# Kernel optimization log

Hardware: AMD Instinct MI355X
Metric: run time of the kernel (lower is better)

The kernel has to match this reference:

```python
import jax, jax.numpy as jnp
import numpy as np

EMBED = 2048
HEADS = 16
HEAD_DIM = EMBED // HEADS


def setup_inputs() -> dict:
    key = jax.random.key(0)
    ks = jax.random.split(key, 9)
    B, S, E = 4, 2048, EMBED
    scale = 1.0 / np.sqrt(E)
    return {
        "values": jax.random.normal(ks[0], (B, S, E), jnp.float32),
        "keys": jax.random.normal(ks[1], (B, S, E), jnp.float32),
        "query": jax.random.normal(ks[2], (B, S, E), jnp.float32),
        "mask": jax.random.randint(ks[3], (1, 1, S, S), 0, 2, jnp.int32),
        "Wv": jax.random.normal(ks[4], (E, E), jnp.float32) * scale,
        "Wk": jax.random.normal(ks[5], (E, E), jnp.float32) * scale,
        "Wq": jax.random.normal(ks[6], (E, E), jnp.float32) * scale,
        "Wo": jax.random.normal(ks[7], (E, E), jnp.float32) * scale,
        "bo": jax.random.normal(ks[8], (E,), jnp.float32) * 0.01,
    }


def reference(values, keys, query, mask, Wv, Wk, Wq, Wo, bo):
    N, q_len, E = query.shape
    # QKV projections (no bias)
    v = jnp.matmul(values, Wv)
    k = jnp.matmul(keys, Wk)
    q = jnp.matmul(query, Wq)
    # [N, len, E] -> [N, heads, len, head_dim]
    def split_heads(x):
        return jnp.transpose(x.reshape(N, x.shape[1], HEADS, HEAD_DIM), (0, 2, 1, 3))
    v, k, q = split_heads(v), split_heads(k), split_heads(q)
    # scaled dot-product attention: [N, H, q_len, k_len]
    energy = jnp.einsum("bhqd,bhkd->bhqk", q, k) / jnp.sqrt(jnp.float32(HEAD_DIM))
    energy = jnp.where(mask == 0, jnp.float32(-1e20), energy)
    attn = jax.nn.softmax(energy, axis=-1)
    out = jnp.einsum("bhqk,bhkd->bhqd", attn, v)
    out = jnp.transpose(out, (0, 2, 1, 3)).reshape(N, q_len, E)
    return jnp.matmul(out, Wo) + bo
```

## Files before the change

### kernel.cpp

```cpp
#include <hip/hip_runtime.h>
#include <hip/hip_bf16.h>
#include <stdint.h>
#include <math.h>

#define EMB   2048
#define NH    16
#define HD    128
#define BATCH 4
#define SEQ   2048

typedef __bf16 bf16_t;
typedef __bf16 bf16x8 __attribute__((ext_vector_type(8)));
typedef __bf16 bf16x4 __attribute__((ext_vector_type(4)));
typedef float  f32x4  __attribute__((ext_vector_type(4)));
typedef float  f32x16 __attribute__((ext_vector_type(16)));

__device__ inline void gload_lds16(const void* g, void* l) {
  __builtin_amdgcn_global_load_lds(
      (const __attribute__((address_space(1))) uint32_t*)g,
      (__attribute__((address_space(3))) uint32_t*)l, 16, 0, 0);
}

__device__ inline uint32_t pack_bf2(float a, float b) {
  uint16_t lo = __builtin_bit_cast(uint16_t, (bf16_t)a);
  uint16_t hi = __builtin_bit_cast(uint16_t, (bf16_t)b);
  return (uint32_t)lo | ((uint32_t)hi << 16);
}

__device__ inline float ex2(float x) {
#if __has_builtin(__builtin_amdgcn_exp2f)
  return __builtin_amdgcn_exp2f(x);
#else
  float r; asm volatile("v_exp_f32 %0, %1" : "=v"(r) : "v"(x)); return r;
#endif
}

__device__ inline uint32_t sext1(uint32_t x, int b) {
  return (uint32_t)(((int32_t)(x << (31 - b))) >> 31);
}
__device__ inline float andf(float p, uint32_t m) {
  return __builtin_bit_cast(float, __builtin_bit_cast(uint32_t, p) & m);
}


__global__ __launch_bounds__(256) void conv_bf16(const float* __restrict__ x,
                                                 bf16_t* __restrict__ y) {
  size_t t = (size_t)blockIdx.x * 256 + threadIdx.x;
  float4 v = ((const float4*)x)[t];
  bf16x4 o;
  o[0] = (bf16_t)v.x; o[1] = (bf16_t)v.y; o[2] = (bf16_t)v.z; o[3] = (bf16_t)v.w;
  ((bf16x4*)y)[t] = o;
}

__global__ __launch_bounds__(256) void convT_w(const float* __restrict__ W,
                                               bf16_t* __restrict__ Wt) {
  __shared__ float t[32][33];
  int tx = threadIdx.x & 31, ty = threadIdx.x >> 5;
  int nb = blockIdx.x * 32, kb = blockIdx.y * 32;
#pragma unroll
  for (int i = 0; i < 4; ++i)
    t[ty + 8 * i][tx] = W[(size_t)(kb + ty + 8 * i) * EMB + nb + tx];
  __syncthreads();
#pragma unroll
  for (int i = 0; i < 4; ++i)
    Wt[(size_t)(nb + ty + 8 * i) * EMB + kb + tx] = (bf16_t)t[tx][ty + 8 * i];
}

__global__ __launch_bounds__(256) void pack_mask(const int* __restrict__ mask,
                                                 uint32_t* __restrict__ maskb) {
  int t = blockIdx.x * 256 + threadIdx.x;
  int q = t >> 6, w = t & 63;
  const int* row = mask + (size_t)q * SEQ + w * 32;
  uint32_t acc = 0;
#pragma unroll 8
  for (int i = 0; i < 32; ++i) acc |= (row[i] != 0 ? 1u : 0u) << i;
  maskb[t] = acc;
}

#define KTILES (EMB / 64)

template <int MODE>
__global__ __launch_bounds__(512, 2) void gemm256(const bf16_t* __restrict__ A,
                                                  const bf16_t* __restrict__ Bt,
                                                  bf16_t* __restrict__ outb,
                                                  float* __restrict__ outf,
                                                  const float* __restrict__ bias) {
  extern __shared__ bf16_t lds[];
  const int tid = threadIdx.x;
  const int wid = tid >> 6, lane = tid & 63;
  const int wr = wid >> 2;
  const int wcn = wid & 3;
  const int tn = blockIdx.x & 7;
  const int tm = blockIdx.x >> 3;
  const int m0 = tm * 256, n0 = tn * 256;

  f32x4 acc[8][4] = {};
  bf16x8 af0[4][2], af1[4][2], bfrg[4][2];

  const int trow = tid >> 3;
  const int schunk = ((tid & 7) ^ (trow & 7)) * 8;
  const int fr = lane & 15;
  const int l7 = lane & 7;
  const int hi4 = lane >> 4;
  int cslot[2];
  cslot[0] = ((hi4) ^ l7) * 8;
  cslot[1] = ((4 + hi4) ^ l7) * 8;
  const int arow = wr * 128 + fr;
  const int brow = wcn * 64 + fr;

#define STAGE_HALF(DST, SRC)                                                    \
  do {                                                                          \
    gload_lds16((SRC), &lds[(DST) + wid * 512]);                                \
    gload_lds16((SRC) + (size_t)64 * EMB, &lds[(DST) + wid * 512 + 4096]);      \
  } while (0)

#define STAGE_TILE(B, KT)                                                       \
  do {                                                                          \
    const bf16_t* _a = A + (size_t)(m0 + trow) * EMB + (KT) * 64 + schunk;      \
    STAGE_HALF((B) * 16384, _a);                                                \
    STAGE_HALF((B) * 16384 + 8192, _a + (size_t)128 * EMB);                     \
    const bf16_t* _b = Bt + (size_t)(n0 + trow) * EMB + (KT) * 64 + schunk;     \
    STAGE_HALF(32768 + (B) * 16384, _b);                                        \
    STAGE_HALF(32768 + (B) * 16384 + 8192, _b + (size_t)128 * EMB);             \
  } while (0)

#define READ_A(DST, P, QM)                                                      \
  _Pragma("unroll") for (int i = 0; i < 4; ++i)                                 \
  _Pragma("unroll") for (int ks = 0; ks < 2; ++ks)                              \
    DST[i][ks] = *(const bf16x8*)&lds[(P) * 16384 +                             \
                    (arow + ((QM) * 4 + i) * 16) * 64 + cslot[ks]];

#define READ_B_ALL(P)                                                           \
  _Pragma("unroll") for (int nf = 0; nf < 4; ++nf)                              \
  _Pragma("unroll") for (int ks = 0; ks < 2; ++ks)                              \
    bfrg[nf][ks] = *(const bf16x8*)&lds[32768 + (P) * 16384 +                   \
                    (brow + nf * 16) * 64 + cslot[ks]];

#define MFMA_HALF(SRC, QM)                                                      \
    _Pragma("unroll") for (int i = 0; i < 4; ++i)                               \
    _Pragma("unroll") for (int nf = 0; nf < 4; ++nf)                            \
    _Pragma("unroll") for (int ks = 0; ks < 2; ++ks) {                          \
      if (MODE == 1)                                                            \
        acc[(QM) * 4 + i][nf] = __builtin_amdgcn_mfma_f32_16x16x32_bf16(        \
            bfrg[nf][ks], SRC[i][ks], acc[(QM) * 4 + i][nf], 0, 0, 0);          \
      else                                                                      \
        acc[(QM) * 4 + i][nf] = __builtin_amdgcn_mfma_f32_16x16x32_bf16(        \
            SRC[i][ks], bfrg[nf][ks], acc[(QM) * 4 + i][nf], 0, 0, 0);          \
    }

#define ITER_MAIN(T, P)                                                         \
  do {                                                                          \
    READ_B_ALL(P);                                                              \
    READ_A(af0, P, 0);                                                          \
    READ_A(af1, P, 1);                                                          \
    __builtin_amdgcn_s_setprio(1);                                              \
    MFMA_HALF(af0, 0)                                                           \
    MFMA_HALF(af1, 1)                                                           \
    __builtin_amdgcn_s_setprio(0);                                              \
    asm volatile("s_barrier" ::: "memory");                                     \
    STAGE_TILE(P, (T) + 2);                                                     \
    asm volatile("s_waitcnt vmcnt(8)" ::: "memory");                            \
    asm volatile("s_barrier" ::: "memory");                                     \
  } while (0)

#define ITER_TAIL(P, LAST)                                                      \
  do {                                                                          \
    READ_B_ALL(P);                                                              \
    READ_A(af0, P, 0);                                                          \
    READ_A(af1, P, 1);                                                          \
    __builtin_amdgcn_s_setprio(1);                                              \
    MFMA_HALF(af0, 0)                                                           \
    MFMA_HALF(af1, 1)                                                           \
    __builtin_amdgcn_s_setprio(0);                                              \
    if (!(LAST)) {                                                              \
      asm volatile("s_waitcnt vmcnt(0)" ::: "memory");                          \
      asm volatile("s_barrier" ::: "memory");                                   \
    }                                                                           \
  } while (0)

  STAGE_TILE(0, 0);
  STAGE_TILE(1, 1);
  asm volatile("s_waitcnt vmcnt(8)" ::: "memory");
  asm volatile("s_barrier" ::: "memory");

  for (int t = 0; t < KTILES - 2; t += 2) {
    ITER_MAIN(t, 0);
    ITER_MAIN(t + 1, 1);
  }
  ITER_TAIL(0, 0);
  ITER_TAIL(1, 1);
#undef ITER_TAIL
#undef ITER_MAIN
#undef MFMA_HALF
#undef READ_B_ALL
#undef READ_A
#undef STAGE_TILE
#undef STAGE_HALF

  const int col0 = lane & 15;
  const int row0 = (lane >> 4) * 4;
#pragma unroll
  for (int mf = 0; mf < 8; ++mf) {
#pragma unroll
    for (int r = 0; r < 4; ++r) {
#pragma unroll
      for (int nf = 0; nf < 4; ++nf) {
        float v = acc[mf][nf][r];
        if (MODE == 1) {
          int nr = n0 + wcn * 64 + nf * 16 + row0 + r;
          int mc = m0 + wr * 128 + mf * 16 + col0;
          int b = mc >> 11, s = mc & 2047, h = nr >> 7, d = nr & 127;
          outb[((size_t)(b * NH + h) * HD + d) * SEQ + s] = (bf16_t)v;
        } else {
          int m = m0 + wr * 128 + mf * 16 + row0 + r;
          int n = n0 + wcn * 64 + nf * 16 + col0;
          if (MODE == 0) {
            int b = m >> 11, s = m & 2047, h = n >> 7, d = n & 127;
            outb[((size_t)(b * NH + h) * SEQ + s) * HD + d] = (bf16_t)v;
          } else {
            outf[(size_t)m * EMB + n] = v + bias[n];
          }
        }
      }
    }
  }
}

__global__ __launch_bounds__(256, 2) void attn_fwd(const bf16_t* __restrict__ Q,
                                                   const bf16_t* __restrict__ K,
                                                   const bf16_t* __restrict__ Vt,
                                                   const uint32_t* __restrict__ maskb,
                                                   bf16_t* __restrict__ O) {
  __shared__ bf16_t Ks[2][64 * 128];
  __shared__ bf16_t Vs[2][128 * 64];
  const int tid = threadIdx.x;
  const int wid = tid >> 6, lane = tid & 63;
  const int ln = lane & 31, hi = lane >> 5;
  const int bid = blockIdx.x;
  const int slot = bid >> 3;
  const int bh = (bid & 7) * 8 + (slot >> 4);
  const int qt = slot & 15;
  const int b = bh >> 4, h = bh & 15;
  const int q = qt * 128 + wid * 32 + ln;
  const float C2 = 0.08838834764831845f * 1.4426950408889634f;

  bf16x8 qf[8];
  const bf16_t* qrow = Q + ((size_t)bh * SEQ + q) * HD;
#pragma unroll
  for (int ks = 0; ks < 8; ++ks)
    qf[ks] = *(const bf16x8*)&qrow[ks * 16 + hi * 8];

  const bf16_t* kp[8];
  const bf16_t* vp[4];
#pragma unroll
  for (int ks = 0; ks < 8; ++ks)
    kp[ks] = &Ks[0][ln * 128 + (((2 * ks + hi) ^ (ln & 15)) * 8)];
#pragma unroll
  for (int ks = 0; ks < 4; ++ks)
    vp[ks] = &Vs[0][ln * 64 + (((2 * ks + hi) ^ (ln & 7)) * 8)];

  f32x16 oacc[4] = {};
  float mC = -INFINITY, l_run = 0.f;

  const size_t kbase = (size_t)bh * SEQ * HD;
  const size_t vbase = (size_t)bh * HD * SEQ;
  const uint2* mb = (const uint2*)maskb;

#define STAGE(BUF, KT)                                                          \
  do {                                                                          \
    const int _k0 = (KT) * 64;                                                  \
    _Pragma("unroll")                                                           \
    for (int j = 0; j < 4; ++j) {                                               \
      int i = wid * 4 + j;                                                      \
      { int r = i * 4 + (lane >> 4); int c = lane & 15;                         \
        gload_lds16(&K[kbase + (size_t)(_k0 + r) * HD + ((c ^ (r & 15)) * 8)],  \
                    &Ks[BUF][i * 512]); }                                       \
      { int r = i * 8 + (lane >> 3); int c = lane & 7;                          \
        gload_lds16(&Vt[vbase + (size_t)r * SEQ + _k0 + ((c ^ (r & 7)) * 8)],   \
                    &Vs[BUF][i * 512]); }                                       \
    }                                                                           \
  } while (0)

  const int NT = SEQ / 64;
  uint2 mw_cur = mb[(size_t)q * 32];
  uint2 mw_next;
  STAGE(0, 0);

#define TILE(KT, P)                                                             \
  {                                                                             \
    asm volatile("s_waitcnt vmcnt(0)" ::: "memory");                            \
    asm volatile("s_barrier" ::: "memory");                                     \
    if ((KT) + 1 < NT) {                                                        \
      mw_next = mb[(size_t)q * 32 + (KT) + 1];                                  \
      STAGE((P) ^ 1, (KT) + 1);                                                 \
    }                                                                           \
    f32x16 sacc0 = {}, sacc1 = {};                                              \
    __builtin_amdgcn_s_setprio(1);                                              \
    _Pragma("unroll")                                                           \
    for (int ks = 0; ks < 8; ++ks) {                                            \
      bf16x8 kf0 = *(const bf16x8*)(kp[ks] + (P) * 8192);                       \
      bf16x8 kf1 = *(const bf16x8*)(kp[ks] + 4096 + (P) * 8192);                \
      sacc0 = __builtin_amdgcn_mfma_f32_32x32x16_bf16(kf0, qf[ks], sacc0, 0, 0, 0); \
      sacc1 = __builtin_amdgcn_mfma_f32_32x32x16_bf16(kf1, qf[ks], sacc1, 0, 0, 0); \
    }                                                                           \
    __builtin_amdgcn_s_setprio(0);                                              \
    const uint32_t mwx = mw_cur.x >> (4 * hi);                                  \
    const uint32_t mwy = mw_cur.y >> (4 * hi);                                  \
    float pmax = -INFINITY;                                                     \
    _Pragma("unroll")                                                           \
    for (int r = 0; r < 16; r += 4)                                             \
      pmax = fmaxf(pmax, fmaxf(fmaxf(sacc0[r], sacc0[r + 1]),                   \
                               fmaxf(sacc0[r + 2], sacc0[r + 3])));             \
    _Pragma("unroll")                                                           \
    for (int r = 0; r < 16; r += 4)                                             \
      pmax = fmaxf(pmax, fmaxf(fmaxf(sacc1[r], sacc1[r + 1]),                   \
                               fmaxf(sacc1[r + 2], sacc1[r + 3])));             \
    pmax = fmaxf(pmax, __shfl_xor(pmax, 32, 64));                               \
    const float pmaxC = pmax * C2;                                              \
    if (!__all(pmaxC - mC <= 8.0f)) {                                           \
      const float mnewC = fmaxf(mC, pmaxC);                                     \
      const float corr = ex2(mC - mnewC);                                       \
      _Pragma("unroll")                                                         \
      for (int mv = 0; mv < 4; ++mv)                                            \
        _Pragma("unroll")                                                       \
        for (int r = 0; r < 16; ++r) oacc[mv][r] *= corr;                       \
      l_run *= corr;                                                            \
      mC = mnewC;                                                               \
    }                                                                           \
    const float nmC = -mC;                                                      \
    float psum = 0.f;                                                           \
    uint32_t pk[2][4][2];                                                       \
    _Pragma("unroll")                                                           \
    for (int g = 0; g < 4; ++g) {                                               \
      float p0 = andf(ex2(fmaf(sacc0[4 * g + 0], C2, nmC)), sext1(mwx, 8 * g + 0)); \
      float p1 = andf(ex2(fmaf(sacc0[4 * g + 1], C2, nmC)), sext1(mwx, 8 * g + 1)); \
      float p2 = andf(ex2(fmaf(sacc0[4 * g + 2], C2, nmC)), sext1(mwx, 8 * g + 2)); \
      float p3 = andf(ex2(fmaf(sacc0[4 * g + 3], C2, nmC)), sext1(mwx, 8 * g + 3)); \
      psum += (p0 + p1) + (p2 + p3);                                            \
      pk[0][g][0] = pack_bf2(p0, p1);                                           \
      pk[0][g][1] = pack_bf2(p2, p3);                                           \
      float q0 = andf(ex2(fmaf(sacc1[4 * g + 0], C2, nmC)), sext1(mwy, 8 * g + 0)); \
      float q1 = andf(ex2(fmaf(sacc1[4 * g + 1], C2, nmC)), sext1(mwy, 8 * g + 1)); \
      float q2 = andf(ex2(fmaf(sacc1[4 * g + 2], C2, nmC)), sext1(mwy, 8 * g + 2)); \
      float q3 = andf(ex2(fmaf(sacc1[4 * g + 3], C2, nmC)), sext1(mwy, 8 * g + 3)); \
      psum += (q0 + q1) + (q2 + q3);                                            \
      pk[1][g][0] = pack_bf2(q0, q1);                                           \
      pk[1][g][1] = pack_bf2(q2, q3);                                           \
    }                                                                           \
    psum += __shfl_xor(psum, 32, 64);                                           \
    l_run += psum;                                                              \
    _Pragma("unroll")                                                           \
    for (int ks = 0; ks < 4; ++ks) {                                            \
      const int mfp = ks >> 1;                                                  \
      const int gA = (2 * ks) & 3;                                              \
      uint32_t w0 = pk[mfp][gA][0], w1 = pk[mfp][gA][1];                        \
      uint32_t w2 = pk[mfp][gA + 1][0], w3 = pk[mfp][gA + 1][1];                \
      asm("v_permlane32_swap_b32 %0, %1" : "+v"(w0), "+v"(w2));                 \
      asm("v_permlane32_swap_b32 %0, %1" : "+v"(w1), "+v"(w3));                 \
      uint4 bw = make_uint4(w0, w1, w2, w3);                                    \
      bf16x8 pb = __builtin_bit_cast(bf16x8, bw);                               \
      __builtin_amdgcn_s_setprio(1);                                            \
      _Pragma("unroll")                                                         \
      for (int mv = 0; mv < 4; ++mv) {                                          \
        bf16x8 vf = *(const bf16x8*)(vp[ks] + mv * 2048 + (P) * 8192);          \
        oacc[mv] = __builtin_amdgcn_mfma_f32_32x32x16_bf16(vf, pb, oacc[mv], 0, 0, 0); \
      }                                                                         \
      __builtin_amdgcn_s_setprio(0);                                            \
    }                                                                           \
    mw_cur = mw_next;                                                           \
  }

  for (int t = 0; t < NT; t += 2) {
    TILE(t, 0);
    TILE(t + 1, 1);
  }
#undef TILE
#undef STAGE

  const float invl = 1.f / l_run;
  bf16_t* orow = O + ((size_t)b * SEQ + q) * EMB + h * HD;
#pragma unroll
  for (int mv = 0; mv < 4; ++mv) {
#pragma unroll
    for (int g = 0; g < 4; ++g) {
      int d = mv * 32 + 8 * g + 4 * hi;
      bf16x4 ov;
      ov[0] = (bf16_t)(oacc[mv][4 * g + 0] * invl);
      ov[1] = (bf16_t)(oacc[mv][4 * g + 1] * invl);
      ov[2] = (bf16_t)(oacc[mv][4 * g + 2] * invl);
      ov[3] = (bf16_t)(oacc[mv][4 * g + 3] * invl);
      *(bf16x4*)&orow[d] = ov;
    }
  }
}


extern "C" void kernel_launch(void* const* d_in, const int* in_sizes, int n_in,
                              void* d_out, int out_size, void* d_ws, size_t ws_size,
                              hipStream_t stream) {
  const float* values = (const float*)d_in[0];
  const float* keys   = (const float*)d_in[1];
  const float* query  = (const float*)d_in[2];
  const int*   mask   = (const int*)d_in[3];
  const float* Wv = (const float*)d_in[4];
  const float* Wk = (const float*)d_in[5];
  const float* Wq = (const float*)d_in[6];
  const float* Wo = (const float*)d_in[7];
  const float* bo = (const float*)d_in[8];
  float* out = (float*)d_out;

  char* ws = (char*)d_ws;
  bf16_t*   Xbuf  = (bf16_t*)(ws);
  bf16_t*   Wbuf  = (bf16_t*)(ws + 33554432);
  bf16_t*   Qb    = (bf16_t*)(ws + 41943040);
  bf16_t*   Kb    = (bf16_t*)(ws + 75497472);
  bf16_t*   Vtb   = (bf16_t*)(ws + 109051904);
  uint32_t* maskb = (uint32_t*)(ws + 142606336);

  static const size_t GEMM_LDS = 131072;
  hipFuncSetAttribute(reinterpret_cast<const void*>(gemm256<0>),
                      hipFuncAttributeMaxDynamicSharedMemorySize, (int)GEMM_LDS);
  hipFuncSetAttribute(reinterpret_cast<const void*>(gemm256<1>),
                      hipFuncAttributeMaxDynamicSharedMemorySize, (int)GEMM_LDS);
  hipFuncSetAttribute(reinterpret_cast<const void*>(gemm256<2>),
                      hipFuncAttributeMaxDynamicSharedMemorySize, (int)GEMM_LDS);

  dim3 b256(256), b512(512);
  dim3 gconv(16384);
  dim3 gw(64, 64);
  dim3 gg(256);
  dim3 ga(1024);

  pack_mask<<<dim3(512), b256, 0, stream>>>(mask, maskb);

  conv_bf16<<<gconv, b256, 0, stream>>>(query, Xbuf);
  convT_w<<<gw, b256, 0, stream>>>(Wq, Wbuf);
  gemm256<0><<<gg, b512, GEMM_LDS, stream>>>(Xbuf, Wbuf, Qb, nullptr, nullptr);

  conv_bf16<<<gconv, b256, 0, stream>>>(keys, Xbuf);
  convT_w<<<gw, b256, 0, stream>>>(Wk, Wbuf);
  gemm256<0><<<gg, b512, GEMM_LDS, stream>>>(Xbuf, Wbuf, Kb, nullptr, nullptr);

  conv_bf16<<<gconv, b256, 0, stream>>>(values, Xbuf);
  convT_w<<<gw, b256, 0, stream>>>(Wv, Wbuf);
  gemm256<1><<<gg, b512, GEMM_LDS, stream>>>(Xbuf, Wbuf, Vtb, nullptr, nullptr);

  attn_fwd<<<ga, b256, 0, stream>>>(Qb, Kb, Vtb, maskb, Xbuf);

  convT_w<<<gw, b256, 0, stream>>>(Wo, Wbuf);
  gemm256<2><<<gg, b512, GEMM_LDS, stream>>>(Xbuf, Wbuf, nullptr, out, bo);
}
```

Baseline: 525.9 us.

## Process two query sub-tiles per attention block to reuse staged K/V tiles

Each attention workgroup now handles 256 query rows instead of 128: every wave keeps two sets of Q fragments, accumulators and softmax state, and runs the QK/softmax/PV pipeline twice for each staged K/V tile. The grid is halved to 512 blocks. This halves global-to-LDS K/V traffic and barrier count per query, at the cost of roughly doubled accumulator register pressure (two 64-float output accumulators per lane), which may lower occupancy below the 2-blocks-per-CU launch bound or cause spills, and there are fewer blocks to fill the GPU.

```diff
diff --git a/kernel.cpp b/kernel.cpp
--- a/kernel.cpp
+++ b/kernel.cpp
@@ -238,17 +238,21 @@
   const int ln = lane & 31, hi = lane >> 5;
   const int bid = blockIdx.x;
   const int slot = bid >> 3;
-  const int bh = (bid & 7) * 8 + (slot >> 4);
-  const int qt = slot & 15;
+  const int bh = (bid & 7) * 8 + (slot >> 3);
+  const int qt = slot & 7;
   const int b = bh >> 4, h = bh & 15;
-  const int q = qt * 128 + wid * 32 + ln;
+  const int qa = qt * 256 + wid * 32 + ln;
+  const int qb = qa + 128;
   const float C2 = 0.08838834764831845f * 1.4426950408889634f;
 
-  bf16x8 qf[8];
-  const bf16_t* qrow = Q + ((size_t)bh * SEQ + q) * HD;
-#pragma unroll
-  for (int ks = 0; ks < 8; ++ks)
-    qf[ks] = *(const bf16x8*)&qrow[ks * 16 + hi * 8];
+  bf16x8 qfa[8], qfb[8];
+  const bf16_t* qra = Q + ((size_t)bh * SEQ + qa) * HD;
+  const bf16_t* qrb = Q + ((size_t)bh * SEQ + qb) * HD;
+#pragma unroll
+  for (int ks = 0; ks < 8; ++ks) {
+    qfa[ks] = *(const bf16x8*)&qra[ks * 16 + hi * 8];
+    qfb[ks] = *(const bf16x8*)&qrb[ks * 16 + hi * 8];
+  }
 
   const bf16_t* kp[8];
   const bf16_t* vp[4];
@@ -259,8 +263,9 @@
   for (int ks = 0; ks < 4; ++ks)
     vp[ks] = &Vs[0][ln * 64 + (((2 * ks + hi) ^ (ln & 7)) * 8)];
 
-  f32x16 oacc[4] = {};
-  float mC = -INFINITY, l_run = 0.f;
+  f32x16 oaccA[4] = {}, oaccB[4] = {};
+  float mCA = -INFINITY, lA = 0.f;
+  float mCB = -INFINITY, lB = 0.f;
 
   const size_t kbase = (size_t)bh * SEQ * HD;
   const size_t vbase = (size_t)bh * HD * SEQ;
@@ -282,30 +287,25 @@
   } while (0)
 
   const int NT = SEQ / 64;
-  uint2 mw_cur = mb[(size_t)q * 32];
-  uint2 mw_next;
+  uint2 mwA_cur = mb[(size_t)qa * 32];
+  uint2 mwB_cur = mb[(size_t)qb * 32];
+  uint2 mwA_next, mwB_next;
   STAGE(0, 0);
 
-#define TILE(KT, P)                                                             \
+#define SUBTILE(P, QF, OACC, MC, LR, MW)                                        \
   {                                                                             \
-    asm volatile("s_waitcnt vmcnt(0)" ::: "memory");                            \
-    asm volatile("s_barrier" ::: "memory");                                     \
-    if ((KT) + 1 < NT) {                                                        \
-      mw_next = mb[(size_t)q * 32 + (KT) + 1];                                  \
-      STAGE((P) ^ 1, (KT) + 1);                                                 \
-    }                                                                           \
     f32x16 sacc0 = {}, sacc1 = {};                                              \
     __builtin_amdgcn_s_setprio(1);                                              \
     _Pragma("unroll")                                                           \
     for (int ks = 0; ks < 8; ++ks) {                                            \
       bf16x8 kf0 = *(const bf16x8*)(kp[ks] + (P) * 8192);                       \
       bf16x8 kf1 = *(const bf16x8*)(kp[ks] + 4096 + (P) * 8192);                \
-      sacc0 = __builtin_amdgcn_mfma_f32_32x32x16_bf16(kf0, qf[ks], sacc0, 0, 0, 0); \
-      sacc1 = __builtin_amdgcn_mfma_f32_32x32x16_bf16(kf1, qf[ks], sacc1, 0, 0, 0); \
+      sacc0 = __builtin_amdgcn_mfma_f32_32x32x16_bf16(kf0, QF[ks], sacc0, 0, 0, 0); \
+      sacc1 = __builtin_amdgcn_mfma_f32_32x32x16_bf16(kf1, QF[ks], sacc1, 0, 0, 0); \
     }                                                                           \
     __builtin_amdgcn_s_setprio(0);                                              \
-    const uint32_t mwx = mw_cur.x >> (4 * hi);                                  \
-    const uint32_t mwy = mw_cur.y >> (4 * hi);                                  \
+    const uint32_t mwx = (MW).x >> (4 * hi);                                    \
+    const uint32_t mwy = (MW).y >> (4 * hi);                                    \
     float pmax = -INFINITY;                                                     \
     _Pragma("unroll")                                                           \
     for (int r = 0; r < 16; r += 4)                                             \
@@ -317,17 +317,17 @@
                                fmaxf(sacc1[r + 2], sacc1[r + 3])));             \
     pmax = fmaxf(pmax, __shfl_xor(pmax, 32, 64));                               \
     const float pmaxC = pmax * C2;                                              \
-    if (!__all(pmaxC - mC <= 8.0f)) {                                           \
-      const float mnewC = fmaxf(mC, pmaxC);                                     \
-      const float corr = ex2(mC - mnewC);                                       \
+    if (!__all(pmaxC - (MC) <= 8.0f)) {                                         \
+      const float mnewC = fmaxf((MC), pmaxC);                                   \
+      const float corr = ex2((MC) - mnewC);                                     \
       _Pragma("unroll")                                                         \
       for (int mv = 0; mv < 4; ++mv)                                            \
         _Pragma("unroll")                                                       \
-        for (int r = 0; r < 16; ++r) oacc[mv][r] *= corr;                       \
-      l_run *= corr;                                                            \
-      mC = mnewC;                                                               \
-    }                                                                           \
-    const float nmC = -mC;                                                      \
+        for (int r = 0; r < 16; ++r) OACC[mv][r] *= corr;                       \
+      (LR) *= corr;                                                             \
+      (MC) = mnewC;                                                             \
+    }                                                                           \
+    const float nmC = -(MC);                                                    \
     float psum = 0.f;                                                           \
     uint32_t pk[2][4][2];                                                       \
     _Pragma("unroll")                                                           \
@@ -348,7 +348,7 @@
       pk[1][g][1] = pack_bf2(q2, q3);                                           \
     }                                                                           \
     psum += __shfl_xor(psum, 32, 64);                                           \
-    l_run += psum;                                                              \
+    (LR) += psum;                                                               \
     _Pragma("unroll")                                                           \
     for (int ks = 0; ks < 4; ++ks) {                                            \
       const int mfp = ks >> 1;                                                  \
@@ -363,11 +363,25 @@
       _Pragma("unroll")                                                         \
       for (int mv = 0; mv < 4; ++mv) {                                          \
         bf16x8 vf = *(const bf16x8*)(vp[ks] + mv * 2048 + (P) * 8192);          \
-        oacc[mv] = __builtin_amdgcn_mfma_f32_32x32x16_bf16(vf, pb, oacc[mv], 0, 0, 0); \
+        OACC[mv] = __builtin_amdgcn_mfma_f32_32x32x16_bf16(vf, pb, OACC[mv], 0, 0, 0); \
       }                                                                         \
       __builtin_amdgcn_s_setprio(0);                                            \
     }                                                                           \
-    mw_cur = mw_next;                                                           \
+  }
+
+#define TILE(KT, P)                                                             \
+  {                                                                             \
+    asm volatile("s_waitcnt vmcnt(0)" ::: "memory");                            \
+    asm volatile("s_barrier" ::: "memory");                                     \
+    if ((KT) + 1 < NT) {                                                        \
+      mwA_next = mb[(size_t)qa * 32 + (KT) + 1];                                \
+      mwB_next = mb[(size_t)qb * 32 + (KT) + 1];                                \
+      STAGE((P) ^ 1, (KT) + 1);                                                 \
+    }                                                                           \
+    SUBTILE(P, qfa, oaccA, mCA, lA, mwA_cur)                                    \
+    SUBTILE(P, qfb, oaccB, mCB, lB, mwB_cur)                                    \
+    mwA_cur = mwA_next;                                                         \
+    mwB_cur = mwB_next;                                                         \
   }
 
   for (int t = 0; t < NT; t += 2) {
@@ -375,21 +389,29 @@
     TILE(t + 1, 1);
   }
 #undef TILE
+#undef SUBTILE
 #undef STAGE
 
-  const float invl = 1.f / l_run;
-  bf16_t* orow = O + ((size_t)b * SEQ + q) * EMB + h * HD;
+  const float invlA = 1.f / lA;
+  const float invlB = 1.f / lB;
+  bf16_t* orowA = O + ((size_t)b * SEQ + qa) * EMB + h * HD;
+  bf16_t* orowB = O + ((size_t)b * SEQ + qb) * EMB + h * HD;
 #pragma unroll
   for (int mv = 0; mv < 4; ++mv) {
 #pragma unroll
     for (int g = 0; g < 4; ++g) {
       int d = mv * 32 + 8 * g + 4 * hi;
-      bf16x4 ov;
-      ov[0] = (bf16_t)(oacc[mv][4 * g + 0] * invl);
-      ov[1] = (bf16_t)(oacc[mv][4 * g + 1] * invl);
-      ov[2] = (bf16_t)(oacc[mv][4 * g + 2] * invl);
-      ov[3] = (bf16_t)(oacc[mv][4 * g + 3] * invl);
-      *(bf16x4*)&orow[d] = ov;
+      bf16x4 ova, ovb;
+      ova[0] = (bf16_t)(oaccA[mv][4 * g + 0] * invlA);
+      ova[1] = (bf16_t)(oaccA[mv][4 * g + 1] * invlA);
+      ova[2] = (bf16_t)(oaccA[mv][4 * g + 2] * invlA);
+      ova[3] = (bf16_t)(oaccA[mv][4 * g + 3] * invlA);
+      *(bf16x4*)&orowA[d] = ova;
+      ovb[0] = (bf16_t)(oaccB[mv][4 * g + 0] * invlB);
+      ovb[1] = (bf16_t)(oaccB[mv][4 * g + 1] * invlB);
+      ovb[2] = (bf16_t)(oaccB[mv][4 * g + 2] * invlB);
+      ovb[3] = (bf16_t)(oaccB[mv][4 * g + 3] * invlB);
+      *(bf16x4*)&orowB[d] = ovb;
     }
   }
 }
@@ -429,7 +451,7 @@
   dim3 gconv(16384);
   dim3 gw(64, 64);
   dim3 gg(256);
-  dim3 ga(1024);
+  dim3 ga(512);
 
   pack_mask<<<dim3(512), b256, 0, stream>>>(mask, maskb);
 
```

After: 770.3 us. +46.5%, slower.
